# Optimization experiments

Measured on AMD Instinct MI355X. Metric: run time of the kernel, lower is better.

Reference implementation:

```python
import jax, jax.numpy as jnp
import numpy as np

DIM = 384
HEADS = 12
WS = 7


def setup_inputs() -> dict:
    key = jax.random.key(0)
    ks = jax.random.split(key, 5)
    B, H, W = 16, 56, 56
    x = jax.random.normal(ks[0], (B, H * W, DIM), dtype=jnp.float32)
    # torch Linear weight (out,in) used as x @ W here, qkv_bias=False
    w_qkv = jax.random.normal(ks[1], (DIM, 3 * DIM), dtype=jnp.float32) * 0.02
    w_proj = jax.random.normal(ks[2], (DIM, DIM), dtype=jnp.float32) * 0.02
    b_proj = jax.random.normal(ks[3], (DIM,), dtype=jnp.float32) * 0.02
    # depthwise 3x3 conv (groups=dim): HWIO kernel (3,3,1,DIM), bias=True
    w_conv = jax.random.normal(ks[4], (3, 3, 1, DIM), dtype=jnp.float32) * 0.02
    b_conv = jnp.zeros((DIM,), jnp.float32)
    return {"x": x, "w_qkv": w_qkv, "w_proj": w_proj, "b_proj": b_proj,
            "w_conv": w_conv, "b_conv": b_conv, "H": H, "W": W}


def reference(x, w_qkv, w_proj, b_proj, w_conv, b_conv, H, W):
    B, N, C = x.shape
    hd = C // HEADS
    scale = hd ** (-0.5)
    hg, wg = H // WS, W // WS  # H,W chosen divisible by ws (no-pad fast path)

    qkv = x @ w_qkv  # (B, N, 3C)
    q, k, v = jnp.split(qkv, 3, axis=-1)

    def to_win(t):
        # (B,N,C) -> (B, n_windows, heads, ws*ws, head_dim)
        t = t.reshape(B, hg, WS, wg, WS, HEADS, hd)
        return t.transpose(0, 1, 3, 5, 2, 4, 6).reshape(B, hg * wg, HEADS, WS * WS, hd)

    qw, kw, vw = to_win(q), to_win(k), to_win(v)

    attn = jax.nn.softmax(jnp.einsum('bwhqd,bwhkd->bwhqk', qw, kw) * scale, axis=-1)
    out = jnp.einsum('bwhqk,bwhkd->bwhqd', attn, vw)
    # merge windows back: (B,nw,heads,q,d) -> (B,N,C)
    out = out.reshape(B, hg, wg, HEADS, WS, WS, hd)
    out = out.transpose(0, 1, 4, 2, 5, 3, 6).reshape(B, N, C)

    # LIM: win2img(img2win(v)) is just v as (B,C,H,W); depthwise 3x3 conv
    v_img = v.reshape(B, H, W, C).transpose(0, 3, 1, 2)
    v_lim = jax.lax.conv_general_dilated(
        v_img, w_conv, window_strides=(1, 1), padding='SAME',
        dimension_numbers=('NCHW', 'HWIO', 'NCHW'), feature_group_count=C)
    v_lim = v_lim + b_conv[None, :, None, None]
    v_lim = v_lim.reshape(B, C, N).transpose(0, 2, 1)  # (B, N, C)

    out = out + v_lim
    return out @ w_proj + b_proj
```

## Files before the change

### kernel.cpp

```cpp
#include <hip/hip_runtime.h>
#include <cstdint>
#include <cstddef>

typedef __bf16 bf16x8 __attribute__((ext_vector_type(8)));
typedef float floatx4 __attribute__((ext_vector_type(4)));

#define DEV static __device__ __forceinline__

DEV float bf2f(uint16_t u) {
    union { uint32_t i; float f; } x; x.i = ((uint32_t)u) << 16; return x.f;
}
DEV uint16_t f2bf(float f) {
    uint32_t u = __float_as_uint(f);
    uint32_t r = (u + 0x7FFFu + ((u >> 16) & 1u)) >> 16;
    return (uint16_t)r;
}
DEV bf16x8 as_bf8(uint4 u) {
    union { uint4 u; bf16x8 b; } c; c.u = u; return c.b;
}
DEV void g2l16(const void* g, void* l) {
    __builtin_amdgcn_global_load_lds(
        (const __attribute__((address_space(1))) void*)g,
        (__attribute__((address_space(3))) void*)l, 16, 0, 0);
}

union U16x8 { uint16_t h[8]; uint4 u; };

constexpr int DIMC  = 384;
constexpr int HEADS = 12;
constexpr int IMH   = 56, IMW = 56;
constexpr int NTOK  = IMH * IMW;
constexpr int BATCH = 16;
constexpr int MTOT  = BATCH * NTOK;
constexpr int QKVLD = 3 * DIMC;
constexpr int GK    = 384;

__global__ __launch_bounds__(256) void cvt_bf16(const float* __restrict__ in,
                                                uint16_t* __restrict__ out)
{
    size_t i = ((size_t)blockIdx.x * 256 + threadIdx.x) * 8;
    float4 a = *(const float4*)(in + i);
    float4 b = *(const float4*)(in + i + 4);
    U16x8 t;
    t.h[0] = f2bf(a.x); t.h[1] = f2bf(a.y); t.h[2] = f2bf(a.z); t.h[3] = f2bf(a.w);
    t.h[4] = f2bf(b.x); t.h[5] = f2bf(b.y); t.h[6] = f2bf(b.z); t.h[7] = f2bf(b.w);
    *(uint4*)(out + i) = t.u;
}

__global__ __launch_bounds__(256) void transpose_cvt(const float* __restrict__ in,
                                                     uint16_t* __restrict__ out,
                                                     int R, int C)
{
    int idx = blockIdx.x * 256 + threadIdx.x;
    int r = idx % R, c = idx / R;
    out[idx] = f2bf(in[(size_t)r * C + c]);
}

template<bool CF32>
__global__ __launch_bounds__(256) void gemm_bt(const uint16_t* __restrict__ A,
                                               const uint16_t* __restrict__ Bt,
                                               const float* __restrict__ bias,
                                               void* __restrict__ Cptr,
                                               int N)
{
    __shared__ __align__(16) uint16_t sA[2][128 * 32];
    __shared__ __align__(16) uint16_t sB[2][128 * 32];

    const int t    = threadIdx.x;
    const int NB   = N >> 7;
    const int bid  = blockIdx.x;
    const int chunk = bid / (8 * NB);
    const int r     = bid % (8 * NB);
    const int bm    = chunk * 8 + (r & 7);
    const int bn    = r >> 3;
    const int wave = t >> 6, lane = t & 63;
    const int wm   = (wave >> 1) * 64, wn = (wave & 1) * 64;
    const int lr   = lane & 15, quad = lane >> 4;

    const uint16_t* Ag = A  + (size_t)(bm * 128 + (t >> 2)) * GK + (t & 3) * 8;
    const uint16_t* Bg = Bt + (size_t)(bn * 128 + (t >> 2)) * GK + (t & 3) * 8;

    auto stage = [&](int buf, int k0) {
        g2l16(Ag + k0, sA[buf] + wave * 512);
        g2l16(Ag + (size_t)64 * GK + k0, sA[buf] + 2048 + wave * 512);
        g2l16(Bg + k0, sB[buf] + wave * 512);
        g2l16(Bg + (size_t)64 * GK + k0, sB[buf] + 2048 + wave * 512);
    };

    floatx4 acc[4][4] = {};

    stage(0, 0);
    __syncthreads();

    #pragma unroll
    for (int ks = 0; ks < 12; ++ks) {
        const int cur = ks & 1;
        if (ks < 11) stage(cur ^ 1, (ks + 1) * 32);

        bf16x8 af[4], bfr[4];
        #pragma unroll
        for (int mt = 0; mt < 4; ++mt)
            af[mt] = *(const bf16x8*)&sA[cur][(wm + mt * 16 + lr) * 32 + quad * 8];
        #pragma unroll
        for (int nt = 0; nt < 4; ++nt)
            bfr[nt] = *(const bf16x8*)&sB[cur][(wn + nt * 16 + lr) * 32 + quad * 8];
        #pragma unroll
        for (int mt = 0; mt < 4; ++mt)
            #pragma unroll
            for (int nt = 0; nt < 4; ++nt)
                acc[mt][nt] = __builtin_amdgcn_mfma_f32_16x16x32_bf16(
                    af[mt], bfr[nt], acc[mt][nt], 0, 0, 0);

        __syncthreads();
    }

    #pragma unroll
    for (int mt = 0; mt < 4; ++mt) {
        #pragma unroll
        for (int nt = 0; nt < 4; ++nt) {
            int gc = bn * 128 + wn + nt * 16 + lr;
            float bv = bias ? bias[gc] : 0.0f;
            int gr0 = bm * 128 + wm + mt * 16 + quad * 4;
            #pragma unroll
            for (int i = 0; i < 4; ++i) {
                if constexpr (CF32) {
                    ((float*)Cptr)[(size_t)(gr0 + i) * N + gc] = acc[mt][nt][i] + bv;
                } else {
                    ((uint16_t*)Cptr)[(size_t)(gr0 + i) * N + gc] = f2bf(acc[mt][nt][i] + bv);
                }
            }
        }
    }
}

constexpr int PLD = 72;
constexpr int WAVE_ELEMS = (64 + 32) * PLD + 81 * 32;

__global__ __launch_bounds__(128) void attn_mfma(const uint16_t* __restrict__ qkv,
                                                 const float* __restrict__ wconv,
                                                 const float* __restrict__ bconv,
                                                 uint16_t* __restrict__ y)
{
    __shared__ uint16_t lds[2][WAVE_ELEMS];
    __shared__ float    warr_all[2][320];

    const int wave = threadIdx.x >> 6;
    const int lane = threadIdx.x & 63;
    const int unit = blockIdx.x * 2 + wave;
    const int h  = unit % HEADS;
    const int w  = (unit / HEADS) & 63;
    const int b  = unit / (HEADS * 64);
    const int wy = w >> 3, wx = w & 7;
    const int lr = lane & 15, quad = lane >> 4;

    uint16_t* Pbuf  = lds[wave];
    uint16_t* Vt    = lds[wave] + 64 * PLD;
    uint16_t* Vhalo = lds[wave] + 96 * PLD;
    float*    warr  = warr_all[wave];

    #pragma unroll
    for (int it = 0; it < 5; ++it) {
        int idx = it * 64 + lane;
        if (idx < 288) warr[idx] = wconv[(idx >> 5) * DIMC + h * 32 + (idx & 31)];
    }
    if (lane < 32) warr[288 + lane] = bconv[h * 32 + lane];

    #pragma unroll
    for (int it = 0; it < 6; ++it) {
        int u = it * 16 + (lane >> 2);
        int g = lane & 3;
        if (u < 81) {
            int hy = u / 9, hx = u % 9;
            int iy = wy * 7 + hy - 1, ix = wx * 7 + hx - 1;
            uint4 val{0, 0, 0, 0};
            if (iy >= 0 && iy < IMH && ix >= 0 && ix < IMW)
                val = *(const uint4*)(qkv + (size_t)(b * NTOK + iy * IMW + ix) * QKVLD
                                      + 2 * DIMC + h * 32 + g * 8);
            *(uint4*)&Vhalo[u * 32 + g * 8] = val;
        }
    }

    auto rowbase = [&](int i, int which) -> const uint16_t* {
        int py = i / 7, px = i % 7;
        int n = (wy * 7 + py) * IMW + wx * 7 + px;
        return qkv + (size_t)(b * NTOK + n) * QKVLD + which * DIMC + h * 32;
    };

    uint4 qf[4], kf[4];
    #pragma unroll
    for (int tm = 0; tm < 4; ++tm) {
        int i = tm * 16 + lr;
        if (i < 49) {
            qf[tm] = *(const uint4*)(rowbase(i, 0) + quad * 8);
            kf[tm] = *(const uint4*)(rowbase(i, 1) + quad * 8);
        } else {
            qf[tm] = uint4{0, 0, 0, 0};
            kf[tm] = uint4{0, 0, 0, 0};
        }
    }

    {
        int j = lane;
        if (j < 49) {
            int hrow = (j / 7 + 1) * 9 + (j % 7 + 1);
            #pragma unroll
            for (int p = 0; p < 4; ++p) {
                U16x8 tmp; tmp.u = *(const uint4*)&Vhalo[hrow * 32 + p * 8];
                #pragma unroll
                for (int q = 0; q < 8; ++q) Vt[(p * 8 + q) * PLD + j] = tmp.h[q];
            }
        } else {
            #pragma unroll
            for (int d = 0; d < 32; ++d) Vt[d * PLD + j] = 0;
        }
    }

    floatx4 S[4][4] = {};
    #pragma unroll
    for (int tm = 0; tm < 4; ++tm)
        #pragma unroll
        for (int tn = 0; tn < 4; ++tn)
            S[tm][tn] = __builtin_amdgcn_mfma_f32_16x16x32_bf16(
                as_bf8(qf[tm]), as_bf8(kf[tn]), S[tm][tn], 0, 0, 0);

    const float scale = 0.17677669529663687f;
    const bool v3 = (lr == 0);
    #pragma unroll
    for (int tm = 0; tm < 4; ++tm) {
        #pragma unroll
        for (int i = 0; i < 4; ++i) {
            float e0 = __expf(S[tm][0][i] * scale);
            float e1 = __expf(S[tm][1][i] * scale);
            float e2 = __expf(S[tm][2][i] * scale);
            float e3 = v3 ? __expf(S[tm][3][i] * scale) : 0.0f;
            float s = e0 + e1 + e2 + e3;
            #pragma unroll
            for (int d = 1; d < 16; d <<= 1) s += __shfl_xor(s, d);
            float inv = 1.0f / s;
            int row = tm * 16 + quad * 4 + i;
            Pbuf[row * PLD + lr]      = f2bf(e0 * inv);
            Pbuf[row * PLD + 16 + lr] = f2bf(e1 * inv);
            Pbuf[row * PLD + 32 + lr] = f2bf(e2 * inv);
            Pbuf[row * PLD + 48 + lr] = f2bf(e3 * inv);
        }
    }

    floatx4 O[4][2] = {};
    #pragma unroll
    for (int kk = 0; kk < 2; ++kk) {
        bf16x8 pf[4], vf[2];
        #pragma unroll
        for (int tm = 0; tm < 4; ++tm)
            pf[tm] = *(const bf16x8*)&Pbuf[(tm * 16 + lr) * PLD + kk * 32 + quad * 8];
        #pragma unroll
        for (int tn = 0; tn < 2; ++tn)
            vf[tn] = *(const bf16x8*)&Vt[(tn * 16 + lr) * PLD + kk * 32 + quad * 8];
        #pragma unroll
        for (int tm = 0; tm < 4; ++tm)
            #pragma unroll
            for (int tn = 0; tn < 2; ++tn)
                O[tm][tn] = __builtin_amdgcn_mfma_f32_16x16x32_bf16(
                    pf[tm], vf[tn], O[tm][tn], 0, 0, 0);
    }

    uint16_t* convb = Vt;
    #pragma unroll
    for (int it = 0; it < 4; ++it) {
        int u = it * 64 + lane;
        if (u < 196) {
            int j = u >> 2, g = u & 3;
            int py = j / 7, px = j % 7;
            float acc[8];
            {
                float4 b0 = *(const float4*)(warr + 288 + g * 8);
                float4 b1 = *(const float4*)(warr + 288 + g * 8 + 4);
                acc[0] = b0.x; acc[1] = b0.y; acc[2] = b0.z; acc[3] = b0.w;
                acc[4] = b1.x; acc[5] = b1.y; acc[6] = b1.z; acc[7] = b1.w;
            }
            #pragma unroll
            for (int ky = 0; ky < 3; ++ky) {
                #pragma unroll
                for (int kx = 0; kx < 3; ++kx) {
                    int hrow = (py + ky) * 9 + (px + kx);
                    U16x8 v; v.u = *(const uint4*)&Vhalo[hrow * 32 + g * 8];
                    const float* wp = warr + (ky * 3 + kx) * 32 + g * 8;
                    float4 w0 = *(const float4*)wp;
                    float4 w1 = *(const float4*)(wp + 4);
                    acc[0] += bf2f(v.h[0]) * w0.x;
                    acc[1] += bf2f(v.h[1]) * w0.y;
                    acc[2] += bf2f(v.h[2]) * w0.z;
                    acc[3] += bf2f(v.h[3]) * w0.w;
                    acc[4] += bf2f(v.h[4]) * w1.x;
                    acc[5] += bf2f(v.h[5]) * w1.y;
                    acc[6] += bf2f(v.h[6]) * w1.z;
                    acc[7] += bf2f(v.h[7]) * w1.w;
                }
            }
            U16x8 r;
            #pragma unroll
            for (int q = 0; q < 8; ++q) r.h[q] = f2bf(acc[q]);
            *(uint4*)&convb[j * 32 + g * 8] = r.u;
        }
    }

    #pragma unroll
    for (int tm = 0; tm < 4; ++tm) {
        #pragma unroll
        for (int i = 0; i < 4; ++i) {
            int r = tm * 16 + quad * 4 + i;
            if (r < 49) {
                int py = r / 7, px = r % 7;
                int n = (wy * 7 + py) * IMW + wx * 7 + px;
                uint16_t* dst = y + (size_t)(b * NTOK + n) * DIMC + h * 32;
                float c0 = bf2f(convb[r * 32 + lr]);
                float c1 = bf2f(convb[r * 32 + 16 + lr]);
                dst[lr]      = f2bf(O[tm][0][i] + c0);
                dst[16 + lr] = f2bf(O[tm][1][i] + c1);
            }
        }
    }
}

extern "C" void kernel_launch(void* const* d_in, const int* in_sizes, int n_in,
                              void* d_out, int out_size, void* d_ws, size_t ws_size,
                              hipStream_t stream)
{
    const float* x      = (const float*)d_in[0];
    const float* w_qkv  = (const float*)d_in[1];
    const float* w_proj = (const float*)d_in[2];
    const float* b_proj = (const float*)d_in[3];
    const float* w_conv = (const float*)d_in[4];
    const float* b_conv = (const float*)d_in[5];
    float* out = (float*)d_out;

    char* ws = (char*)d_ws;
    uint16_t* qkv    = (uint16_t*)ws;
    uint16_t* xb     = (uint16_t*)(ws + 115605504);
    uint16_t* yb     = xb;
    uint16_t* wqkvT  = (uint16_t*)(ws + 115605504 + 38535168);
    uint16_t* wprojT = wqkvT + QKVLD * GK;

    cvt_bf16<<<dim3((MTOT * DIMC) / (8 * 256)), 256, 0, stream>>>(x, xb);
    transpose_cvt<<<dim3((GK * QKVLD) / 256), 256, 0, stream>>>(w_qkv, wqkvT, GK, QKVLD);
    transpose_cvt<<<dim3((GK * DIMC) / 256), 256, 0, stream>>>(w_proj, wprojT, GK, DIMC);

    gemm_bt<false><<<dim3((MTOT / 128) * (QKVLD / 128)), 256, 0, stream>>>(
        xb, wqkvT, nullptr, qkv, QKVLD);

    attn_mfma<<<dim3(BATCH * 64 * HEADS / 2), 128, 0, stream>>>(
        qkv, w_conv, b_conv, yb);

    gemm_bt<true><<<dim3((MTOT / 128) * (DIMC / 128)), 256, 0, stream>>>(
        yb, wprojT, b_proj, out, DIMC);
}
```

Before: 320.2 us.

## Compute transposed attention scores and keep softmax probabilities in registers

```diff
diff --git a/kernel.cpp b/kernel.cpp
--- a/kernel.cpp
+++ b/kernel.cpp
@@ -134,7 +134,7 @@
 }
 
 constexpr int PLD = 72;
-constexpr int WAVE_ELEMS = (64 + 32) * PLD + 81 * 32;
+constexpr int WAVE_ELEMS = 32 * PLD + 81 * 32;
 
 __global__ __launch_bounds__(128) void attn_mfma(const uint16_t* __restrict__ qkv,
                                                  const float* __restrict__ wconv,
@@ -153,9 +153,8 @@
     const int wy = w >> 3, wx = w & 7;
     const int lr = lane & 15, quad = lane >> 4;
 
-    uint16_t* Pbuf  = lds[wave];
-    uint16_t* Vt    = lds[wave] + 64 * PLD;
-    uint16_t* Vhalo = lds[wave] + 96 * PLD;
+    uint16_t* Vt    = lds[wave];
+    uint16_t* Vhalo = lds[wave] + 32 * PLD;
     float*    warr  = warr_all[wave];
 
     #pragma unroll
@@ -217,50 +216,81 @@
 
     floatx4 S[4][4] = {};
     #pragma unroll
-    for (int tm = 0; tm < 4; ++tm)
-        #pragma unroll
-        for (int tn = 0; tn < 4; ++tn)
-            S[tm][tn] = __builtin_amdgcn_mfma_f32_16x16x32_bf16(
-                as_bf8(qf[tm]), as_bf8(kf[tn]), S[tm][tn], 0, 0, 0);
+    for (int ta = 0; ta < 4; ++ta)
+        #pragma unroll
+        for (int tb = 0; tb < 4; ++tb)
+            S[ta][tb] = __builtin_amdgcn_mfma_f32_16x16x32_bf16(
+                as_bf8(kf[ta]), as_bf8(qf[tb]), S[ta][tb], 0, 0, 0);
 
     const float scale = 0.17677669529663687f;
-    const bool v3 = (lr == 0);
-    #pragma unroll
-    for (int tm = 0; tm < 4; ++tm) {
-        #pragma unroll
-        for (int i = 0; i < 4; ++i) {
-            float e0 = __expf(S[tm][0][i] * scale);
-            float e1 = __expf(S[tm][1][i] * scale);
-            float e2 = __expf(S[tm][2][i] * scale);
-            float e3 = v3 ? __expf(S[tm][3][i] * scale) : 0.0f;
-            float s = e0 + e1 + e2 + e3;
-            #pragma unroll
-            for (int d = 1; d < 16; d <<= 1) s += __shfl_xor(s, d);
-            float inv = 1.0f / s;
-            int row = tm * 16 + quad * 4 + i;
-            Pbuf[row * PLD + lr]      = f2bf(e0 * inv);
-            Pbuf[row * PLD + 16 + lr] = f2bf(e1 * inv);
-            Pbuf[row * PLD + 32 + lr] = f2bf(e2 * inv);
-            Pbuf[row * PLD + 48 + lr] = f2bf(e3 * inv);
-        }
-    }
-
-    floatx4 O[4][2] = {};
+    float psum[4] = {0.f, 0.f, 0.f, 0.f};
+    #pragma unroll
+    for (int ta = 0; ta < 4; ++ta) {
+        #pragma unroll
+        for (int tb = 0; tb < 4; ++tb) {
+            #pragma unroll
+            for (int i = 0; i < 4; ++i) {
+                float e;
+                if (ta < 3) e = __expf(S[ta][tb][i] * scale);
+                else        e = (quad == 0 && i == 0)
+                                ? __expf(S[ta][tb][i] * scale) : 0.0f;
+                S[ta][tb][i] = e;
+                psum[tb] += e;
+            }
+        }
+    }
+    #pragma unroll
+    for (int tb = 0; tb < 4; ++tb) {
+        float s = psum[tb];
+        s += __shfl_xor(s, 16);
+        s += __shfl_xor(s, 32);
+        psum[tb] = 1.0f / s;
+    }
+
+    uint32_t pkv[4][4][2];
+    #pragma unroll
+    for (int ta = 0; ta < 4; ++ta) {
+        #pragma unroll
+        for (int tb = 0; tb < 4; ++tb) {
+            #pragma unroll
+            for (int hh = 0; hh < 2; ++hh) {
+                float lo = S[ta][tb][2 * hh]     * psum[tb];
+                float hi = S[ta][tb][2 * hh + 1] * psum[tb];
+                asm("v_cvt_pk_bf16_f32 %0, %1, %2"
+                    : "=v"(pkv[ta][tb][hh]) : "v"(lo), "v"(hi));
+            }
+        }
+    }
+
+    const int lo_lane = (quad & 1) * 32 + lr;
+    const bool hiq = quad >= 2;
+    floatx4 Ot[2][4] = {};
     #pragma unroll
     for (int kk = 0; kk < 2; ++kk) {
-        bf16x8 pf[4], vf[2];
-        #pragma unroll
-        for (int tm = 0; tm < 4; ++tm)
-            pf[tm] = *(const bf16x8*)&Pbuf[(tm * 16 + lr) * PLD + kk * 32 + quad * 8];
-        #pragma unroll
-        for (int tn = 0; tn < 2; ++tn)
-            vf[tn] = *(const bf16x8*)&Vt[(tn * 16 + lr) * PLD + kk * 32 + quad * 8];
-        #pragma unroll
-        for (int tm = 0; tm < 4; ++tm)
-            #pragma unroll
-            for (int tn = 0; tn < 2; ++tn)
-                O[tm][tn] = __builtin_amdgcn_mfma_f32_16x16x32_bf16(
-                    pf[tm], vf[tn], O[tm][tn], 0, 0, 0);
+        uint4 pfr[4];
+        #pragma unroll
+        for (int tb = 0; tb < 4; ++tb) {
+            uint32_t a0 = (uint32_t)__shfl((int)pkv[kk * 2][tb][0],     lo_lane);
+            uint32_t b0 = (uint32_t)__shfl((int)pkv[kk * 2 + 1][tb][0], lo_lane);
+            uint32_t a1 = (uint32_t)__shfl((int)pkv[kk * 2][tb][1],     lo_lane);
+            uint32_t b1 = (uint32_t)__shfl((int)pkv[kk * 2 + 1][tb][1], lo_lane);
+            uint32_t a2 = (uint32_t)__shfl((int)pkv[kk * 2][tb][0],     lo_lane + 16);
+            uint32_t b2 = (uint32_t)__shfl((int)pkv[kk * 2 + 1][tb][0], lo_lane + 16);
+            uint32_t a3 = (uint32_t)__shfl((int)pkv[kk * 2][tb][1],     lo_lane + 16);
+            uint32_t b3 = (uint32_t)__shfl((int)pkv[kk * 2 + 1][tb][1], lo_lane + 16);
+            pfr[tb] = uint4{hiq ? b0 : a0, hiq ? b1 : a1,
+                            hiq ? b2 : a2, hiq ? b3 : a3};
+        }
+        bf16x8 vf[2];
+        #pragma unroll
+        for (int td = 0; td < 2; ++td)
+            vf[td] = *(const bf16x8*)&Vt[(td * 16 + lr) * PLD + kk * 32 + quad * 8];
+        #pragma unroll
+        for (int td = 0; td < 2; ++td)
+            #pragma unroll
+            for (int tb = 0; tb < 4; ++tb)
+                Ot[td][tb] = __builtin_amdgcn_mfma_f32_16x16x32_bf16(
+                    vf[td], as_bf8(pfr[tb]), Ot[td][tb], 0, 0, 0);
     }
 
     uint16_t* convb = Vt;
@@ -296,26 +326,32 @@
                     acc[7] += bf2f(v.h[7]) * w1.w;
                 }
             }
-            U16x8 r;
-            #pragma unroll
-            for (int q = 0; q < 8; ++q) r.h[q] = f2bf(acc[q]);
-            *(uint4*)&convb[j * 32 + g * 8] = r.u;
-        }
-    }
-
-    #pragma unroll
-    for (int tm = 0; tm < 4; ++tm) {
-        #pragma unroll
-        for (int i = 0; i < 4; ++i) {
-            int r = tm * 16 + quad * 4 + i;
-            if (r < 49) {
-                int py = r / 7, px = r % 7;
-                int n = (wy * 7 + py) * IMW + wx * 7 + px;
-                uint16_t* dst = y + (size_t)(b * NTOK + n) * DIMC + h * 32;
-                float c0 = bf2f(convb[r * 32 + lr]);
-                float c1 = bf2f(convb[r * 32 + 16 + lr]);
-                dst[lr]      = f2bf(O[tm][0][i] + c0);
-                dst[16 + lr] = f2bf(O[tm][1][i] + c1);
+            U16x8 rr;
+            #pragma unroll
+            for (int q = 0; q < 8; ++q) rr.h[q] = f2bf(acc[q]);
+            *(uint4*)&convb[j * 32 + g * 8] = rr.u;
+        }
+    }
+
+    #pragma unroll
+    for (int tb = 0; tb < 4; ++tb) {
+        int q = tb * 16 + lr;
+        if (q < 49) {
+            int py = q / 7, px = q % 7;
+            int n = (wy * 7 + py) * IMW + wx * 7 + px;
+            uint16_t* dst = y + (size_t)(b * NTOK + n) * DIMC + h * 32;
+            #pragma unroll
+            for (int td = 0; td < 2; ++td) {
+                int d0 = td * 16 + quad * 4;
+                uint2 cv = *(const uint2*)&convb[q * 32 + d0];
+                float o0 = Ot[td][tb][0] + bf2f((uint16_t)(cv.x & 0xffffu));
+                float o1 = Ot[td][tb][1] + bf2f((uint16_t)(cv.x >> 16));
+                float o2 = Ot[td][tb][2] + bf2f((uint16_t)(cv.y & 0xffffu));
+                float o3 = Ot[td][tb][3] + bf2f((uint16_t)(cv.y >> 16));
+                uint32_t w0, w1;
+                asm("v_cvt_pk_bf16_f32 %0, %1, %2" : "=v"(w0) : "v"(o0), "v"(o1));
+                asm("v_cvt_pk_bf16_f32 %0, %1, %2" : "=v"(w1) : "v"(o2), "v"(o3));
+                *(uint2*)(dst + d0) = uint2{w0, w1};
             }
         }
     }
```

Result: faster. 307.5 us (-4.0%).
